# Kernel optimization log

Hardware: AMD Instinct MI355X
Metric: run time of the kernel (lower is better)

The kernel has to match this reference:

```python
import jax, jax.numpy as jnp
import numpy as np

B, S = 4, 16384
D_IN, D_HID, D_KEY, D_VAL, N_HEADS = 512, 2048, 64, 64, 8
SEG_FULL, SAMP = 2048, 4
SEG = SEG_FULL // SAMP  # 512: MoD capacity per segment, also attn segment_len


def setup_inputs() -> dict:
    key = jax.random.key(0)
    ks = jax.random.split(key, 10)
    sc = lambda i, shape: (jax.random.normal(ks[i], shape, jnp.float32) * 0.02)
    return {
        "x": jax.random.normal(ks[0], (B, S, D_IN), jnp.float32),
        "w_samp": sc(1, (D_IN, 1)), "b_samp": jnp.zeros((1,), jnp.float32),
        "w_q": sc(2, (D_IN, N_HEADS * D_KEY)),
        "w_k": sc(3, (D_IN, N_HEADS * D_KEY)),
        "w_v": sc(4, (D_IN, N_HEADS * D_VAL)),
        "w_o": sc(5, (N_HEADS * D_VAL, D_IN)),
        "betas": jax.random.normal(ks[6], (1, N_HEADS, 1, D_VAL), jnp.float32),
        "w1": sc(7, (D_IN, D_HID)), "b1": jnp.zeros((D_HID,), jnp.float32),
        "w2": sc(8, (D_HID, D_IN)), "b2": jnp.zeros((D_IN,), jnp.float32),
    }


def _cm_attention(x, w_q, w_k, w_v, w_o, betas):
    """CompressiveMemory: segment-recurrent linear-attn memory + local softmax attn."""
    b, n, _ = x.shape
    nseg = n // SEG

    def split(w, dh):
        y = (x @ w).reshape(b, n, N_HEADS, dh).transpose(0, 2, 1, 3)          # [b,H,n,dh]
        return y.reshape(b, N_HEADS, nseg, SEG, dh).transpose(2, 0, 1, 3, 4)  # [nseg,b,H,SEG,dh]

    qs, ks_, vs = split(w_q, D_KEY), split(w_k, D_KEY), split(w_v, D_VAL)
    gate = jax.nn.sigmoid(betas)                                              # [1,H,1,dv]
    mem0 = jnp.zeros((b, N_HEADS, D_KEY, D_VAL), x.dtype)
    z0 = jnp.ones((b, N_HEADS, D_KEY, 1), x.dtype) / D_KEY
    scale = D_KEY ** -0.5

    def step(carry, seg):
        mem, z = carry
        q, k, v = seg
        sq = jax.nn.elu(q) + 1.0
        sk = jax.nn.elu(k) + 1.0
        scores = jnp.einsum('bhqk,bhsk->bhqs', q, k) * scale
        att_dot = jax.nn.softmax(scores, axis=-1) @ v                         # [b,H,SEG,dv]
        att_mem = (sq @ mem) / (sq @ z)                                       # uses pre-update mem,z
        mem = mem + jnp.einsum('bhsk,bhsv->bhkv', sk, v)                      # linear update
        z = z + sk.sum(axis=-2)[..., None]
        att = gate * att_mem + (1.0 - gate) * att_dot
        return (mem, z), att

    _, outs = jax.lax.scan(step, (mem0, z0), (qs, ks_, vs))                   # [nseg,b,H,SEG,dv]
    out = outs.transpose(1, 0, 3, 2, 4).reshape(b, n, N_HEADS * D_VAL)
    return out @ w_o


def reference(x, w_samp, b_samp, w_q, w_k, w_v, w_o, betas, w1, b1, w2, b2):
    b, s, d = x.shape
    nseg = s // SEG_FULL
    scores = (x @ w_samp + b_samp)[..., 0]                                    # [B,S]
    # top-SEG tokens per full segment (training-mode routing), kept in sequence order
    seg_scores = scores.reshape(b, nseg, SEG_FULL)
    top = jnp.argsort(-seg_scores, axis=-1)[:, :, :SEG]                       # [B,nseg,SEG]
    sel = jnp.sort(top, axis=-1) + (jnp.arange(nseg) * SEG_FULL)[None, :, None]
    flat = sel.reshape(b, nseg * SEG)                                         # global indices, [B,Ssel]
    x_sel = jnp.take_along_axis(x, flat[..., None], axis=1)                   # gather [B,Ssel,D]
    h = _cm_attention(x_sel, w_q, w_k, w_v, w_o, betas)
    h = jax.nn.gelu(h @ w1 + b1, approximate=False) @ w2 + b2                 # MLP (dropout=0)
    bi = jnp.arange(b)[:, None]
    x_out = x.at[bi, flat].add(h)                                             # scatter-add back
    mask = jnp.zeros((b, s), x.dtype).at[bi, flat].set(1.0)
    # faithful to source: zero positions >= number of selected tokens
    pad = (jnp.arange(s)[None, :] < mask.sum(axis=1)[:, None]).astype(x.dtype)
    x_out = x_out * pad[..., None]
    return x_out, mask.reshape(-1, 1), scores.reshape(-1, 1)
```

## Files before the change

### kernel.cpp

```cpp
#include <hip/hip_runtime.h>
#include <math.h>

#define S_TOT 16384
#define BATCH 4
#define DIN 512
#define NH 8
#define DK 64
#define SEGF 2048
#define SEGS 512
#define NSEG 8
#define NUSE 2
#define MROWS (BATCH*NUSE*SEGS)

typedef unsigned int u32;
typedef __attribute__((ext_vector_type(8))) short short8;
typedef __attribute__((ext_vector_type(4))) float f32x4;

__device__ __forceinline__ short f2b(float f) {
  u32 u = __float_as_uint(f);
  u32 r = u + 0x7fffu + ((u >> 16) & 1u);
  return (short)(r >> 16);
}
__device__ __forceinline__ float b2f(short s) {
  return __uint_as_float(((u32)(unsigned short)s) << 16);
}
__device__ __forceinline__ float b2f_lo(u32 u) { return __uint_as_float(u << 16); }
__device__ __forceinline__ float b2f_hi(u32 u) { return __uint_as_float(u & 0xffff0000u); }

__global__ __launch_bounds__(256) void scores_kernel(
    const float* __restrict__ x, const float* __restrict__ w,
    const float* __restrict__ bsamp, float* __restrict__ out)
{
  int tok  = blockIdx.x * 4 + (threadIdx.x >> 6);
  int lane = threadIdx.x & 63;
  const float4* xr = (const float4*)(x + (size_t)tok * DIN);
  const float4* wr = (const float4*)w;
  float4 a0 = xr[lane],      w0 = wr[lane];
  float4 a1 = xr[lane + 64], w1v = wr[lane + 64];
  float p = a0.x*w0.x + a0.y*w0.y + a0.z*w0.z + a0.w*w0.w
          + a1.x*w1v.x + a1.y*w1v.y + a1.z*w1v.z + a1.w*w1v.w;
  #pragma unroll
  for (int off = 32; off > 0; off >>= 1) p += __shfl_down(p, off);
  if (lane == 0) out[tok] = p + bsamp[0];
}

__global__ __launch_bounds__(256) void topk_rank(
    const float* __restrict__ scores, int* __restrict__ flags,
    float* __restrict__ maskOut)
{
  int c = blockIdx.x & 7, g = (blockIdx.x >> 3) & 7, b = blockIdx.x >> 6;
  __shared__ float sc[SEGF];
  int tid = threadIdx.x;
  const float* src = scores + (size_t)b*S_TOT + (size_t)g*SEGF;
  *(float4*)&sc[tid*8]     = *(const float4*)(src + tid*8);
  *(float4*)&sc[tid*8 + 4] = *(const float4*)(src + tid*8 + 4);
  __syncthreads();
  int i0 = c*256 + tid;
  float mine = sc[i0];
  int cnt = 0;
  #pragma unroll 2
  for (int j = 0; j < SEGF; j += 8) {
    float4 a = *(const float4*)&sc[j];
    float4 d = *(const float4*)&sc[j + 4];
    cnt += (a.x > mine || (a.x == mine && (j+0) < i0)) ? 1 : 0;
    cnt += (a.y > mine || (a.y == mine && (j+1) < i0)) ? 1 : 0;
    cnt += (a.z > mine || (a.z == mine && (j+2) < i0)) ? 1 : 0;
    cnt += (a.w > mine || (a.w == mine && (j+3) < i0)) ? 1 : 0;
    cnt += (d.x > mine || (d.x == mine && (j+4) < i0)) ? 1 : 0;
    cnt += (d.y > mine || (d.y == mine && (j+5) < i0)) ? 1 : 0;
    cnt += (d.z > mine || (d.z == mine && (j+6) < i0)) ? 1 : 0;
    cnt += (d.w > mine || (d.w == mine && (j+7) < i0)) ? 1 : 0;
  }
  int flg = (cnt < SEGS) ? 1 : 0;
  flags[(((b << 3) + g) << 11) + i0] = flg;
  maskOut[(size_t)b*S_TOT + (size_t)g*SEGF + i0] = flg ? 1.0f : 0.0f;
}

__global__ __launch_bounds__(256) void topk_compact(
    const int* __restrict__ flags, int* __restrict__ flat, int* __restrict__ inv)
{
  int g = blockIdx.x & 1, b = blockIdx.x >> 1;
  __shared__ int wsum[4];
  int tid = threadIdx.x;
  int lane = tid & 63, w = tid >> 6;
  const int* f = flags + (((b << 3) + g) << 11);
  int fl[8]; int ls = 0;
  #pragma unroll
  for (int l = 0; l < 8; ++l) { fl[l] = f[tid*8 + l]; ls += fl[l]; }
  int inc = ls;
  #pragma unroll
  for (int off = 1; off < 64; off <<= 1) {
    int t = __shfl_up(inc, off);
    if (lane >= off) inc += t;
  }
  if (lane == 63) wsum[w] = inc;
  __syncthreads();
  int base = 0;
  #pragma unroll
  for (int ww = 0; ww < 4; ++ww) base += (ww < w) ? wsum[ww] : 0;
  int pos = base + inc - ls;
  #pragma unroll
  for (int l = 0; l < 8; ++l) {
    int i = tid*8 + l;
    inv[b*(NUSE*SEGF) + g*SEGF + i] = fl[l] ? (g*SEGS + pos) : -1;
    if (fl[l]) {
      flat[b*(NSEG*SEGS) + g*SEGS + pos] = g*SEGF + i;
      pos++;
    }
  }
}

__global__ __launch_bounds__(256) void transpose_all(
    const float* __restrict__ w_q, const float* __restrict__ w_k,
    const float* __restrict__ w_v, const float* __restrict__ w_o,
    const float* __restrict__ w1,  const float* __restrict__ w2,
    short* __restrict__ Wtqkv, short* __restrict__ Wto,
    short* __restrict__ Wt1,   short* __restrict__ Wt2)
{
  __shared__ float t[32][33];
  int bid = blockIdx.x;
  const float* src; short* dst; int K, N, rowoff, tIdx;
  if (bid < 1024) {
    K = 512; N = 512; tIdx = bid & 255;
    int which = bid >> 8;
    src = which == 0 ? w_q : which == 1 ? w_k : which == 2 ? w_v : w_o;
    dst = which == 3 ? Wto : Wtqkv;
    rowoff = which == 3 ? 0 : which * 512;
  } else if (bid < 2048) {
    K = 512; N = 2048; tIdx = bid - 1024; src = w1; dst = Wt1; rowoff = 0;
  } else {
    K = 2048; N = 512; tIdx = bid - 2048; src = w2; dst = Wt2; rowoff = 0;
  }
  int ntN = N >> 5;
  int n0 = (tIdx % ntN) * 32, k0 = (tIdx / ntN) * 32;
  int tid = threadIdx.x;
  int txx = tid & 31, ty = tid >> 5;
  #pragma unroll
  for (int r = 0; r < 4; ++r)
    t[ty + 8*r][txx] = src[(size_t)(k0 + ty + 8*r) * N + n0 + txx];
  __syncthreads();
  #pragma unroll
  for (int r = 0; r < 4; ++r)
    dst[(size_t)(rowoff + n0 + ty + 8*r) * K + k0 + txx] = f2b(t[txx][ty + 8*r]);
}

__global__ __launch_bounds__(256) void gather_cast(
    const float* __restrict__ x, const int* __restrict__ flat,
    short* __restrict__ xsel)
{
  int tok  = blockIdx.x * 4 + (threadIdx.x >> 6);
  int lane = threadIdx.x & 63;
  int b = tok >> 10, i = tok & 1023;
  int gidx = flat[b * (NSEG*SEGS) + i];
  const float* srcp = x + ((size_t)(b * S_TOT + gidx)) * DIN + lane*8;
  float4 a0 = *(const float4*)srcp;
  float4 a1 = *(const float4*)(srcp + 4);
  uint4 o;
  o.x = (u32)(unsigned short)f2b(a0.x) | ((u32)(unsigned short)f2b(a0.y) << 16);
  o.y = (u32)(unsigned short)f2b(a0.z) | ((u32)(unsigned short)f2b(a0.w) << 16);
  o.z = (u32)(unsigned short)f2b(a1.x) | ((u32)(unsigned short)f2b(a1.y) << 16);
  o.w = (u32)(unsigned short)f2b(a1.z) | ((u32)(unsigned short)f2b(a1.w) << 16);
  *(uint4*)(xsel + (size_t)tok * DIN + lane*8) = o;
}

template<int BM, int BN, int WM, int WN>
__global__ __launch_bounds__(256) void gemm_bf16(
    const short* __restrict__ A, const short* __restrict__ Bt,
    const float* __restrict__ bias, float* __restrict__ Cf,
    short* __restrict__ Cb, short* __restrict__ VtOut, short* __restrict__ KtOut,
    int M, int N, int K, int act)
{
  constexpr int BK = 32;
  constexpr int WAVES_N = BN / WN;
  constexpr int FM = WM / 16, FN = WN / 16;
  __shared__ short Al[2][BM * BK];
  __shared__ short Bl[2][BN * BK];
  const int tid = threadIdx.x;
  const int lane = tid & 63, wid = tid >> 6;
  const int wr = wid / WAVES_N, wc = wid % WAVES_N;
  const int bm = blockIdx.y * BM, bn = blockIdx.x * BN;
  const int srow = tid >> 2;
  const int scol = (tid & 3) * 8;

  f32x4 acc[FM][FN];
  #pragma unroll
  for (int i = 0; i < FM; ++i)
    #pragma unroll
    for (int j = 0; j < FN; ++j)
      #pragma unroll
      for (int e = 0; e < 4; ++e) acc[i][j][e] = 0.f;

  const int NT = K / BK;

  auto stage = [&](int t, int buf) {
    const int k0 = t * BK;
    #pragma unroll
    for (int i = 0; i < BM/64; ++i) {
      const short* gp = A + (size_t)(bm + i*64 + srow) * K + k0 + scol;
      __builtin_amdgcn_global_load_lds(
          (const __attribute__((address_space(1))) void*)gp,
          (__attribute__((address_space(3))) void*)&Al[buf][(i*64 + srow)*BK + scol],
          16, 0, 0);
    }
    #pragma unroll
    for (int i = 0; i < BN/64; ++i) {
      const short* gp = Bt + (size_t)(bn + i*64 + srow) * K + k0 + scol;
      __builtin_amdgcn_global_load_lds(
          (const __attribute__((address_space(1))) void*)gp,
          (__attribute__((address_space(3))) void*)&Bl[buf][(i*64 + srow)*BK + scol],
          16, 0, 0);
    }
  };

  stage(0, 0);
  __syncthreads();
  int cur = 0;
  for (int t = 0; t < NT; ++t) {
    if (t + 1 < NT) stage(t + 1, cur ^ 1);
    short8 af[FM], bf_[FN];
    #pragma unroll
    for (int fm = 0; fm < FM; ++fm)
      af[fm] = *(const short8*)&Al[cur][(wr*WM + fm*16 + (lane & 15))*BK + (lane >> 4)*8];
    #pragma unroll
    for (int fn = 0; fn < FN; ++fn)
      bf_[fn] = *(const short8*)&Bl[cur][(wc*WN + fn*16 + (lane & 15))*BK + (lane >> 4)*8];
    #pragma unroll
    for (int fm = 0; fm < FM; ++fm)
      #pragma unroll
      for (int fn = 0; fn < FN; ++fn)
        acc[fm][fn] = __builtin_amdgcn_mfma_f32_16x16x32_bf16(af[fm], bf_[fn], acc[fm][fn], 0, 0, 0);
    __syncthreads();
    cur ^= 1;
  }

  const int crow0 = (lane >> 4) * 4, ccol = lane & 15;
  #pragma unroll
  for (int fm = 0; fm < FM; ++fm) {
    #pragma unroll
    for (int fn = 0; fn < FN; ++fn) {
      int c = bn + wc*WN + fn*16 + ccol;
      int r0 = bm + wr*WM + fm*16 + crow0;
      float vv[4];
      #pragma unroll
      for (int j = 0; j < 4; ++j) {
        float v = acc[fm][fn][j];
        if (bias) v += bias[c];
        if (act == 1) v = 0.5f * v * (1.0f + erff(v * 0.70710678118f));
        vv[j] = v;
        if (Cf) Cf[(size_t)(r0 + j) * N + c] = v;
        if (Cb) Cb[(size_t)(r0 + j) * N + c] = f2b(v);
      }
      if (VtOut && c >= 1024) {
        int hh = (c - 1024) >> 6, dv = c & 63;
        int bb = r0 >> 10, key = r0 & 1023;
        u32 lo = (u32)(unsigned short)f2b(vv[0]) | ((u32)(unsigned short)f2b(vv[1]) << 16);
        u32 hi = (u32)(unsigned short)f2b(vv[2]) | ((u32)(unsigned short)f2b(vv[3]) << 16);
        *(uint2*)&VtOut[((size_t)((bb*8 + hh)*64 + dv) << 10) + key] = make_uint2(lo, hi);
      }
      if (KtOut && c >= 512 && c < 1024) {
        int hh = (c - 512) >> 6, dk = c & 63;
        int bb = r0 >> 10, key = r0 & 1023;
        float e0 = vv[0] > 0.f ? vv[0] + 1.f : __expf(vv[0]);
        float e1 = vv[1] > 0.f ? vv[1] + 1.f : __expf(vv[1]);
        float e2 = vv[2] > 0.f ? vv[2] + 1.f : __expf(vv[2]);
        float e3 = vv[3] > 0.f ? vv[3] + 1.f : __expf(vv[3]);
        u32 lo = (u32)(unsigned short)f2b(e0) | ((u32)(unsigned short)f2b(e1) << 16);
        u32 hi = (u32)(unsigned short)f2b(e2) | ((u32)(unsigned short)f2b(e3) << 16);
        *(uint2*)&KtOut[((size_t)((bb*8 + hh)*64 + dk) << 10) + key] = make_uint2(lo, hi);
      }
    }
  }
}

__global__ __launch_bounds__(256) void memsum_mfma(
    const short* __restrict__ Kt, const short* __restrict__ Vt,
    short* __restrict__ m0t, float* __restrict__ zf)
{
  int b = blockIdx.x >> 3, h = blockIdx.x & 7;
  const short* ktb = Kt + ((size_t)((b*8+h)*64) << 10);
  const short* vtb = Vt + ((size_t)((b*8+h)*64) << 10);
  int tid = threadIdx.x, lane = tid & 63, w = tid >> 6;
  int ln15 = lane & 15, hi8 = (lane >> 4) * 8;
  f32x4 acc[4];
  #pragma unroll
  for (int nf = 0; nf < 4; ++nf) acc[nf] = (f32x4){0.f,0.f,0.f,0.f};
  #pragma unroll 4
  for (int ks = 0; ks < 16; ++ks) {
    short8 a = *(const short8*)&vtb[(size_t)(w*16 + ln15)*1024 + ks*32 + hi8];
    #pragma unroll
    for (int nf = 0; nf < 4; ++nf) {
      short8 bfr = *(const short8*)&ktb[(size_t)(nf*16 + ln15)*1024 + ks*32 + hi8];
      acc[nf] = __builtin_amdgcn_mfma_f32_16x16x32_bf16(a, bfr, acc[nf], 0, 0, 0);
    }
  }
  size_t mb = (size_t)(b*NH + h) * 4096;
  #pragma unroll
  for (int nf = 0; nf < 4; ++nf)
    #pragma unroll
    for (int j = 0; j < 4; ++j)
      m0t[mb + (size_t)(w*16 + (lane>>4)*4 + j)*64 + nf*16 + ln15] = f2b(acc[nf][j]);
  int row = tid >> 2, q = tid & 3;
  float zs = 0.f;
  #pragma unroll 4
  for (int i = 0; i < 16; ++i) {
    short8 kv = *(const short8*)&ktb[(size_t)row*1024 + q*128 + i*8];
    #pragma unroll
    for (int e = 0; e < 8; ++e) zs += b2f(kv[e]);
  }
  zs += __shfl_xor(zs, 1); zs += __shfl_xor(zs, 2);
  if (q == 0) zf[(b*8+h)*64 + row] = 0.015625f + zs;
}

__global__ __launch_bounds__(256) void attn4(
    const short* __restrict__ qkv, const short* __restrict__ vt,
    const short* __restrict__ m0t, const float* __restrict__ zf,
    const float* __restrict__ betas, short* __restrict__ att)
{
  __shared__ short Qs[64*64];
  __shared__ short Ks[128*64];
  __shared__ short Vts[64*128];
  __shared__ short Ps[4*16*128];
  __shared__ float zl[64];
  __shared__ float relay[64];
  int tid = threadIdx.x, lane = tid & 63, w = tid >> 6;
  int ln15 = lane & 15, hi8 = (lane >> 4) * 8;
  int bx = blockIdx.x;
  int qt = bx & 7, h = (bx >> 3) & 7, g = (bx >> 6) & 1, b = bx >> 7;
  const int seg0 = b*1024 + g*512;
  const int qbase = seg0 + qt*64;

  {
    const short* qg = qkv + (size_t)qbase*1536 + h*64;
    #pragma unroll
    for (int p = 0; p < 2; ++p) {
      int slot = p*256 + tid;
      int row = slot >> 3;
      int off = ((slot & 7)*8) ^ ((row & 7)*8);
      __builtin_amdgcn_global_load_lds(
        (const __attribute__((address_space(1))) void*)(qg + (size_t)row*1536 + off),
        (__attribute__((address_space(3))) void*)&Qs[slot*8], 16, 0, 0);
    }
  }
  if (g && tid < 16) *(float4*)&zl[tid*4] = *(const float4*)(zf + (size_t)(b*8+h)*64 + tid*4);
  __syncthreads();

  short8 qf[2];
  {
    int row = w*16 + ln15;
    #pragma unroll
    for (int ks = 0; ks < 2; ++ks)
      qf[ks] = *(const short8*)&Qs[row*64 + ((ks*32 + hi8) ^ ((row&7)*8))];
  }

  const short* kg = qkv + (size_t)seg0*1536 + 512 + h*64;
  const short* vg = vt + ((size_t)((b*8+h)*64) << 10) + g*512;
  short* Pw = &Ps[w*2048];

  f32x4 oacc[4];
  #pragma unroll
  for (int nf = 0; nf < 4; ++nf) oacc[nf] = (f32x4){0.f,0.f,0.f,0.f};
  float lsum[4] = {0.f,0.f,0.f,0.f};

  for (int c = 0; c < 4; ++c) {
    __syncthreads();
    #pragma unroll
    for (int p = 0; p < 4; ++p) {
      int slot = p*256 + tid;
      int row = slot >> 3;
      int off = ((slot & 7)*8) ^ ((row & 7)*8);
      __builtin_amdgcn_global_load_lds(
        (const __attribute__((address_space(1))) void*)(kg + (size_t)(c*128 + row)*1536 + off),
        (__attribute__((address_space(3))) void*)&Ks[slot*8], 16, 0, 0);
    }
    #pragma unroll
    for (int p = 0; p < 4; ++p) {
      int slot = p*256 + tid;
      int row = slot >> 4;
      int off = ((slot & 15)*8) ^ ((row & 7)*8);
      __builtin_amdgcn_global_load_lds(
        (const __attribute__((address_space(1))) void*)(vg + ((size_t)row << 10) + c*128 + off),
        (__attribute__((address_space(3))) void*)&Vts[slot*8], 16, 0, 0);
    }
    __syncthreads();

    f32x4 sf[8];
    #pragma unroll
    for (int nf = 0; nf < 8; ++nf) sf[nf] = (f32x4){0.f,0.f,0.f,0.f};
    #pragma unroll
    for (int ks = 0; ks < 2; ++ks)
      #pragma unroll
      for (int nf = 0; nf < 8; ++nf) {
        int row = nf*16 + ln15;
        short8 kb = *(const short8*)&Ks[row*64 + ((ks*32 + hi8) ^ ((row&7)*8))];
        sf[nf] = __builtin_amdgcn_mfma_f32_16x16x32_bf16(qf[ks], kb, sf[nf], 0, 0, 0);
      }
    #pragma unroll
    for (int nf = 0; nf < 8; ++nf)
      #pragma unroll
      for (int j = 0; j < 4; ++j) {
        float p = __expf(sf[nf][j] * 0.125f);
        lsum[j] += p;
        int q = (lane >> 4)*4 + j;
        int key = nf*16 + ln15;
        Pw[q*128 + (key ^ ((q&7)*8))] = f2b(p);
      }
    #pragma unroll
    for (int ks = 0; ks < 4; ++ks) {
      short8 pa = *(const short8*)&Pw[ln15*128 + ((ks*32 + hi8) ^ ((ln15&7)*8))];
      #pragma unroll
      for (int nf = 0; nf < 4; ++nf) {
        int row = nf*16 + ln15;
        short8 vb = *(const short8*)&Vts[row*128 + ((ks*32 + hi8) ^ ((row&7)*8))];
        oacc[nf] = __builtin_amdgcn_mfma_f32_16x16x32_bf16(pa, vb, oacc[nf], 0, 0, 0);
      }
    }
  }

  float linv[4];
  #pragma unroll
  for (int j = 0; j < 4; ++j) {
    float s = lsum[j];
    s += __shfl_xor(s, 1); s += __shfl_xor(s, 2);
    s += __shfl_xor(s, 4); s += __shfl_xor(s, 8);
    linv[j] = 1.f / s;
  }

  f32x4 mfr[4];
  #pragma unroll
  for (int nf = 0; nf < 4; ++nf) mfr[nf] = (f32x4){0.f,0.f,0.f,0.f};
  float dinv[4] = {0.f,0.f,0.f,0.f};
  if (g) {
    __syncthreads();
    const short* mg = m0t + (size_t)(b*8+h)*4096;
    #pragma unroll
    for (int p = 0; p < 2; ++p) {
      int slot = p*256 + tid;
      int row = slot >> 3;
      int off = ((slot & 7)*8) ^ ((row & 7)*8);
      __builtin_amdgcn_global_load_lds(
        (const __attribute__((address_space(1))) void*)(mg + (size_t)row*64 + off),
        (__attribute__((address_space(3))) void*)&Ks[slot*8], 16, 0, 0);
    }
    __syncthreads();
    float sqv[2][8]; short8 sqf[2];
    #pragma unroll
    for (int ks = 0; ks < 2; ++ks)
      #pragma unroll
      for (int e = 0; e < 8; ++e) {
        float f = b2f(qf[ks][e]);
        f = f > 0.f ? f + 1.f : __expf(f);
        sqv[ks][e] = f; sqf[ks][e] = f2b(f);
      }
    float denp = 0.f;
    #pragma unroll
    for (int ks = 0; ks < 2; ++ks)
      #pragma unroll
      for (int e = 0; e < 8; ++e) denp += sqv[ks][e] * zl[ks*32 + hi8 + e];
    denp += __shfl_xor(denp, 16); denp += __shfl_xor(denp, 32);
    if (lane < 16) relay[w*16 + lane] = denp;
    #pragma unroll
    for (int ks = 0; ks < 2; ++ks)
      #pragma unroll
      for (int nf = 0; nf < 4; ++nf) {
        int row = nf*16 + ln15;
        short8 mb_ = *(const short8*)&Ks[row*64 + ((ks*32 + hi8) ^ ((row&7)*8))];
        mfr[nf] = __builtin_amdgcn_mfma_f32_16x16x32_bf16(sqf[ks], mb_, mfr[nf], 0, 0, 0);
      }
    #pragma unroll
    for (int j = 0; j < 4; ++j)
      dinv[j] = 1.f / relay[w*16 + (lane>>4)*4 + j];
  }

  #pragma unroll
  for (int nf = 0; nf < 4; ++nf) {
    float bt = betas[h*64 + nf*16 + ln15];
    float gt = 1.f / (1.f + __expf(-bt));
    #pragma unroll
    for (int j = 0; j < 4; ++j) {
      float ad = oacc[nf][j] * linv[j];
      float v = g ? (gt * mfr[nf][j] * dinv[j] + (1.f - gt) * ad) : (1.f - gt) * ad;
      int qrow = qbase + w*16 + (lane>>4)*4 + j;
      att[(size_t)qrow*512 + h*64 + nf*16 + ln15] = f2b(v);
    }
  }
}

__global__ __launch_bounds__(256) void final_kernel(
    const float* __restrict__ x, const int* __restrict__ inv,
    const float* __restrict__ hm, float* __restrict__ outX)
{
  int row  = blockIdx.x * 4 + (threadIdx.x >> 6);
  int lane = threadIdx.x & 63;
  int b = row >> 14;
  int s = row & (S_TOT - 1);
  size_t base = (size_t)row * DIN + lane * 8;
  if (s >= NUSE * SEGF) {
    float4 z = make_float4(0.f,0.f,0.f,0.f);
    *(float4*)(outX + base)     = z;
    *(float4*)(outX + base + 4) = z;
    return;
  }
  float4 a0 = *(const float4*)(x + base);
  float4 a1 = *(const float4*)(x + base + 4);
  int i = inv[b * (NUSE*SEGF) + s];
  if (i >= 0) {
    size_t hb = (size_t)(b * (NUSE*SEGS) + i) * DIN + lane * 8;
    float4 h0 = *(const float4*)(hm + hb);
    float4 h1 = *(const float4*)(hm + hb + 4);
    a0.x += h0.x; a0.y += h0.y; a0.z += h0.z; a0.w += h0.w;
    a1.x += h1.x; a1.y += h1.y; a1.z += h1.z; a1.w += h1.w;
  }
  *(float4*)(outX + base)     = a0;
  *(float4*)(outX + base + 4) = a1;
}

extern "C" void kernel_launch(void* const* d_in, const int* in_sizes, int n_in,
                              void* d_out, int out_size, void* d_ws, size_t ws_size,
                              hipStream_t stream) {
  (void)in_sizes; (void)n_in; (void)out_size; (void)ws_size;
  const float* x      = (const float*)d_in[0];
  const float* w_samp = (const float*)d_in[1];
  const float* b_samp = (const float*)d_in[2];
  const float* w_q    = (const float*)d_in[3];
  const float* w_k    = (const float*)d_in[4];
  const float* w_v    = (const float*)d_in[5];
  const float* w_o    = (const float*)d_in[6];
  const float* betas  = (const float*)d_in[7];
  const float* w1     = (const float*)d_in[8];
  const float* b1     = (const float*)d_in[9];
  const float* w2     = (const float*)d_in[10];
  const float* b2     = (const float*)d_in[11];

  float* outX      = (float*)d_out;
  float* outMask   = outX + (size_t)BATCH * S_TOT * DIN;
  float* outScores = outMask + (size_t)BATCH * S_TOT;

  char* ws = (char*)d_ws;
  int*   flat  = (int*)(ws);
  int*   inv   = (int*)(ws + 65536);
  int*   flags = (int*)(ws + 131072);
  short* M0t   = (short*)(ws + 393216);
  float* Zf    = (float*)(ws + 655360);
  short* Wtqkv = (short*)(ws + 1048576);
  short* Wto   = (short*)(ws + 2621440);
  short* Wt1   = (short*)(ws + 3145728);
  short* Wt2   = (short*)(ws + 5242880);
  short* xsel  = (short*)(ws + 7340032);
  short* qkv   = (short*)(ws + 11534336);
  short* Vt    = (short*)(ws + 24117248);
  short* attb  = (short*)(ws + 28311552);
  short* R0b   = (short*)(ws + 32505856);
  short* Kt    = (short*)(ws + 36700160);
  short* hidB  = (short*)(ws + 7340032);
  float* Hf    = (float*)(ws + 24117248);

  scores_kernel<<<(BATCH*S_TOT)/4, 256, 0, stream>>>(x, w_samp, b_samp, outScores);
  topk_rank<<<BATCH*NSEG*8, 256, 0, stream>>>(outScores, flags, outMask);
  topk_compact<<<BATCH*NUSE, 256, 0, stream>>>(flags, flat, inv);

  transpose_all<<<3072, 256, 0, stream>>>(w_q, w_k, w_v, w_o, w1, w2,
                                          Wtqkv, Wto, Wt1, Wt2);

  gather_cast<<<MROWS/4, 256, 0, stream>>>(x, flat, xsel);

  gemm_bf16<128,128,64,64><<<dim3(12,32), 256, 0, stream>>>(
      xsel, Wtqkv, nullptr, nullptr, qkv, Vt, Kt, MROWS, 1536, 512, 0);

  memsum_mfma<<<BATCH*NH, 256, 0, stream>>>(Kt, Vt, M0t, Zf);
  attn4<<<512, 256, 0, stream>>>(qkv, Vt, M0t, Zf, betas, attb);

  gemm_bf16<64,64,32,32><<<dim3(8,64), 256, 0, stream>>>(
      attb, Wto, nullptr, nullptr, R0b, nullptr, nullptr, MROWS, 512, 512, 0);
  gemm_bf16<128,128,64,64><<<dim3(16,32), 256, 0, stream>>>(
      R0b, Wt1, b1, nullptr, hidB, nullptr, nullptr, MROWS, 2048, 512, 1);
  gemm_bf16<64,64,32,32><<<dim3(8,64), 256, 0, stream>>>(
      hidB, Wt2, b2, Hf, nullptr, nullptr, nullptr, MROWS, 512, 2048, 0);

  final_kernel<<<(BATCH*S_TOT)/4, 256, 0, stream>>>(x, inv, Hf, outX);
}
```

Before: 247.2 us.

## Merge score and weight-transpose kernels, widen GEMM K-tile, simplify attn Q load

Combines the routing-score kernel and the weight transpose/cast kernel into a single launch that branches on block index, removing one launch and letting both run together. The bf16 GEMM K-tile grows from 32 to 64 with two MFMA sub-steps per tile, so there are fewer barriers and the staging loop changes. The attention kernel now loads Q fragments straight from global memory into registers instead of staging them in LDS, dropping a barrier and some LDS use, and it raises wave priority around the MFMA sections. The larger K-tile doubles GEMM LDS use, which may lower occupancy, and the unswizzled 64-wide LDS rows may cause bank conflicts.

Result: no change. 248.7 us (+0.6%).

```diff
diff --git a/kernel.cpp b/kernel.cpp
--- a/kernel.cpp
+++ b/kernel.cpp
@@ -24,24 +24,55 @@
 __device__ __forceinline__ float b2f(short s) {
   return __uint_as_float(((u32)(unsigned short)s) << 16);
 }
-__device__ __forceinline__ float b2f_lo(u32 u) { return __uint_as_float(u << 16); }
-__device__ __forceinline__ float b2f_hi(u32 u) { return __uint_as_float(u & 0xffff0000u); }
-
-__global__ __launch_bounds__(256) void scores_kernel(
+
+__global__ __launch_bounds__(256) void scores_transpose(
     const float* __restrict__ x, const float* __restrict__ w,
-    const float* __restrict__ bsamp, float* __restrict__ out)
-{
-  int tok  = blockIdx.x * 4 + (threadIdx.x >> 6);
-  int lane = threadIdx.x & 63;
-  const float4* xr = (const float4*)(x + (size_t)tok * DIN);
-  const float4* wr = (const float4*)w;
-  float4 a0 = xr[lane],      w0 = wr[lane];
-  float4 a1 = xr[lane + 64], w1v = wr[lane + 64];
-  float p = a0.x*w0.x + a0.y*w0.y + a0.z*w0.z + a0.w*w0.w
-          + a1.x*w1v.x + a1.y*w1v.y + a1.z*w1v.z + a1.w*w1v.w;
-  #pragma unroll
-  for (int off = 32; off > 0; off >>= 1) p += __shfl_down(p, off);
-  if (lane == 0) out[tok] = p + bsamp[0];
+    const float* __restrict__ bsamp, float* __restrict__ out,
+    const float* __restrict__ w_q, const float* __restrict__ w_k,
+    const float* __restrict__ w_v, const float* __restrict__ w_o,
+    const float* __restrict__ w1,  const float* __restrict__ w2,
+    short* __restrict__ Wtqkv, short* __restrict__ Wto,
+    short* __restrict__ Wt1,   short* __restrict__ Wt2)
+{
+  __shared__ float t[32][33];
+  int tid = threadIdx.x;
+  if (blockIdx.x < 16384) {
+    int tok  = blockIdx.x * 4 + (tid >> 6);
+    int lane = tid & 63;
+    const float4* xr = (const float4*)(x + (size_t)tok * DIN);
+    const float4* wr = (const float4*)w;
+    float4 a0 = xr[lane],      w0 = wr[lane];
+    float4 a1 = xr[lane + 64], w1v = wr[lane + 64];
+    float p = a0.x*w0.x + a0.y*w0.y + a0.z*w0.z + a0.w*w0.w
+            + a1.x*w1v.x + a1.y*w1v.y + a1.z*w1v.z + a1.w*w1v.w;
+    #pragma unroll
+    for (int off = 32; off > 0; off >>= 1) p += __shfl_down(p, off);
+    if (lane == 0) out[tok] = p + bsamp[0];
+    return;
+  }
+  int bid = blockIdx.x - 16384;
+  const float* src; short* dst; int K, N, rowoff, tIdx;
+  if (bid < 1024) {
+    K = 512; N = 512; tIdx = bid & 255;
+    int which = bid >> 8;
+    src = which == 0 ? w_q : which == 1 ? w_k : which == 2 ? w_v : w_o;
+    dst = which == 3 ? Wto : Wtqkv;
+    rowoff = which == 3 ? 0 : which * 512;
+  } else if (bid < 2048) {
+    K = 512; N = 2048; tIdx = bid - 1024; src = w1; dst = Wt1; rowoff = 0;
+  } else {
+    K = 2048; N = 512; tIdx = bid - 2048; src = w2; dst = Wt2; rowoff = 0;
+  }
+  int ntN = N >> 5;
+  int n0 = (tIdx % ntN) * 32, k0 = (tIdx / ntN) * 32;
+  int txx = tid & 31, ty = tid >> 5;
+  #pragma unroll
+  for (int r = 0; r < 4; ++r)
+    t[ty + 8*r][txx] = src[(size_t)(k0 + ty + 8*r) * N + n0 + txx];
+  __syncthreads();
+  #pragma unroll
+  for (int r = 0; r < 4; ++r)
+    dst[(size_t)(rowoff + n0 + ty + 8*r) * K + k0 + txx] = f2b(t[txx][ty + 8*r]);
 }
 
 __global__ __launch_bounds__(256) void topk_rank(
@@ -110,40 +141,6 @@
   }
 }
 
-__global__ __launch_bounds__(256) void transpose_all(
-    const float* __restrict__ w_q, const float* __restrict__ w_k,
-    const float* __restrict__ w_v, const float* __restrict__ w_o,
-    const float* __restrict__ w1,  const float* __restrict__ w2,
-    short* __restrict__ Wtqkv, short* __restrict__ Wto,
-    short* __restrict__ Wt1,   short* __restrict__ Wt2)
-{
-  __shared__ float t[32][33];
-  int bid = blockIdx.x;
-  const float* src; short* dst; int K, N, rowoff, tIdx;
-  if (bid < 1024) {
-    K = 512; N = 512; tIdx = bid & 255;
-    int which = bid >> 8;
-    src = which == 0 ? w_q : which == 1 ? w_k : which == 2 ? w_v : w_o;
-    dst = which == 3 ? Wto : Wtqkv;
-    rowoff = which == 3 ? 0 : which * 512;
-  } else if (bid < 2048) {
-    K = 512; N = 2048; tIdx = bid - 1024; src = w1; dst = Wt1; rowoff = 0;
-  } else {
-    K = 2048; N = 512; tIdx = bid - 2048; src = w2; dst = Wt2; rowoff = 0;
-  }
-  int ntN = N >> 5;
-  int n0 = (tIdx % ntN) * 32, k0 = (tIdx / ntN) * 32;
-  int tid = threadIdx.x;
-  int txx = tid & 31, ty = tid >> 5;
-  #pragma unroll
-  for (int r = 0; r < 4; ++r)
-    t[ty + 8*r][txx] = src[(size_t)(k0 + ty + 8*r) * N + n0 + txx];
-  __syncthreads();
-  #pragma unroll
-  for (int r = 0; r < 4; ++r)
-    dst[(size_t)(rowoff + n0 + ty + 8*r) * K + k0 + txx] = f2b(t[txx][ty + 8*r]);
-}
-
 __global__ __launch_bounds__(256) void gather_cast(
     const float* __restrict__ x, const int* __restrict__ flat,
     short* __restrict__ xsel)
@@ -170,7 +167,7 @@
     short* __restrict__ Cb, short* __restrict__ VtOut, short* __restrict__ KtOut,
     int M, int N, int K, int act)
 {
-  constexpr int BK = 32;
+  constexpr int BK = 64;
   constexpr int WAVES_N = BN / WN;
   constexpr int FM = WM / 16, FN = WN / 16;
   __shared__ short Al[2][BM * BK];
@@ -179,8 +176,7 @@
   const int lane = tid & 63, wid = tid >> 6;
   const int wr = wid / WAVES_N, wc = wid % WAVES_N;
   const int bm = blockIdx.y * BM, bn = blockIdx.x * BN;
-  const int srow = tid >> 2;
-  const int scol = (tid & 3) * 8;
+  const int ln15 = lane & 15, hi8 = (lane >> 4) * 8;
 
   f32x4 acc[FM][FN];
   #pragma unroll
@@ -195,19 +191,23 @@
   auto stage = [&](int t, int buf) {
     const int k0 = t * BK;
     #pragma unroll
-    for (int i = 0; i < BM/64; ++i) {
-      const short* gp = A + (size_t)(bm + i*64 + srow) * K + k0 + scol;
+    for (int i = 0; i < BM/32; ++i) {
+      int slot = i*256 + tid;
+      int row = slot >> 3, col = (slot & 7) * 8;
+      const short* gp = A + (size_t)(bm + row) * K + k0 + col;
       __builtin_amdgcn_global_load_lds(
           (const __attribute__((address_space(1))) void*)gp,
-          (__attribute__((address_space(3))) void*)&Al[buf][(i*64 + srow)*BK + scol],
+          (__attribute__((address_space(3))) void*)&Al[buf][row*BK + col],
           16, 0, 0);
     }
     #pragma unroll
-    for (int i = 0; i < BN/64; ++i) {
-      const short* gp = Bt + (size_t)(bn + i*64 + srow) * K + k0 + scol;
+    for (int i = 0; i < BN/32; ++i) {
+      int slot = i*256 + tid;
+      int row = slot >> 3, col = (slot & 7) * 8;
+      const short* gp = Bt + (size_t)(bn + row) * K + k0 + col;
       __builtin_amdgcn_global_load_lds(
           (const __attribute__((address_space(1))) void*)gp,
-          (__attribute__((address_space(3))) void*)&Bl[buf][(i*64 + srow)*BK + scol],
+          (__attribute__((address_space(3))) void*)&Bl[buf][row*BK + col],
           16, 0, 0);
     }
   };
@@ -217,18 +217,21 @@
   int cur = 0;
   for (int t = 0; t < NT; ++t) {
     if (t + 1 < NT) stage(t + 1, cur ^ 1);
-    short8 af[FM], bf_[FN];
-    #pragma unroll
-    for (int fm = 0; fm < FM; ++fm)
-      af[fm] = *(const short8*)&Al[cur][(wr*WM + fm*16 + (lane & 15))*BK + (lane >> 4)*8];
-    #pragma unroll
-    for (int fn = 0; fn < FN; ++fn)
-      bf_[fn] = *(const short8*)&Bl[cur][(wc*WN + fn*16 + (lane & 15))*BK + (lane >> 4)*8];
-    #pragma unroll
-    for (int fm = 0; fm < FM; ++fm)
+    #pragma unroll
+    for (int ks = 0; ks < 2; ++ks) {
+      short8 af[FM], bf_[FN];
+      #pragma unroll
+      for (int fm = 0; fm < FM; ++fm)
+        af[fm] = *(const short8*)&Al[cur][(wr*WM + fm*16 + ln15)*BK + ks*32 + hi8];
       #pragma unroll
       for (int fn = 0; fn < FN; ++fn)
-        acc[fm][fn] = __builtin_amdgcn_mfma_f32_16x16x32_bf16(af[fm], bf_[fn], acc[fm][fn], 0, 0, 0);
+        bf_[fn] = *(const short8*)&Bl[cur][(wc*WN + fn*16 + ln15)*BK + ks*32 + hi8];
+      #pragma unroll
+      for (int fm = 0; fm < FM; ++fm)
+        #pragma unroll
+        for (int fn = 0; fn < FN; ++fn)
+          acc[fm][fn] = __builtin_amdgcn_mfma_f32_16x16x32_bf16(af[fm], bf_[fn], acc[fm][fn], 0, 0, 0);
+    }
     __syncthreads();
     cur ^= 1;
   }
@@ -316,7 +319,6 @@
     const short* __restrict__ m0t, const float* __restrict__ zf,
     const float* __restrict__ betas, short* __restrict__ att)
 {
-  __shared__ short Qs[64*64];
   __shared__ short Ks[128*64];
   __shared__ short Vts[64*128];
   __shared__ short Ps[4*16*128];
@@ -329,28 +331,13 @@
   const int seg0 = b*1024 + g*512;
   const int qbase = seg0 + qt*64;
 
-  {
-    const short* qg = qkv + (size_t)qbase*1536 + h*64;
-    #pragma unroll
-    for (int p = 0; p < 2; ++p) {
-      int slot = p*256 + tid;
-      int row = slot >> 3;
-      int off = ((slot & 7)*8) ^ ((row & 7)*8);
-      __builtin_amdgcn_global_load_lds(
-        (const __attribute__((address_space(1))) void*)(qg + (size_t)row*1536 + off),
-        (__attribute__((address_space(3))) void*)&Qs[slot*8], 16, 0, 0);
-    }
-  }
-  if (g && tid < 16) *(float4*)&zl[tid*4] = *(const float4*)(zf + (size_t)(b*8+h)*64 + tid*4);
-  __syncthreads();
-
   short8 qf[2];
   {
-    int row = w*16 + ln15;
-    #pragma unroll
-    for (int ks = 0; ks < 2; ++ks)
-      qf[ks] = *(const short8*)&Qs[row*64 + ((ks*32 + hi8) ^ ((row&7)*8))];
-  }
+    const short* qg = qkv + (size_t)(qbase + w*16 + ln15)*1536 + h*64;
+    qf[0] = *(const short8*)(qg + hi8);
+    qf[1] = *(const short8*)(qg + 32 + hi8);
+  }
+  if (g && tid < 16) *(float4*)&zl[tid*4] = *(const float4*)(zf + (size_t)(b*8+h)*64 + tid*4);
 
   const short* kg = qkv + (size_t)seg0*1536 + 512 + h*64;
   const short* vg = vt + ((size_t)((b*8+h)*64) << 10) + g*512;
@@ -386,6 +373,7 @@
     f32x4 sf[8];
     #pragma unroll
     for (int nf = 0; nf < 8; ++nf) sf[nf] = (f32x4){0.f,0.f,0.f,0.f};
+    __builtin_amdgcn_s_setprio(1);
     #pragma unroll
     for (int ks = 0; ks < 2; ++ks)
       #pragma unroll
@@ -394,6 +382,7 @@
         short8 kb = *(const short8*)&Ks[row*64 + ((ks*32 + hi8) ^ ((row&7)*8))];
         sf[nf] = __builtin_amdgcn_mfma_f32_16x16x32_bf16(qf[ks], kb, sf[nf], 0, 0, 0);
       }
+    __builtin_amdgcn_s_setprio(0);
     #pragma unroll
     for (int nf = 0; nf < 8; ++nf)
       #pragma unroll
@@ -404,6 +393,7 @@
         int key = nf*16 + ln15;
         Pw[q*128 + (key ^ ((q&7)*8))] = f2b(p);
       }
+    __builtin_amdgcn_s_setprio(1);
     #pragma unroll
     for (int ks = 0; ks < 4; ++ks) {
       short8 pa = *(const short8*)&Pw[ln15*128 + ((ks*32 + hi8) ^ ((ln15&7)*8))];
@@ -414,6 +404,7 @@
         oacc[nf] = __builtin_amdgcn_mfma_f32_16x16x32_bf16(pa, vb, oacc[nf], 0, 0, 0);
       }
     }
+    __builtin_amdgcn_s_setprio(0);
   }
 
   float linv[4];
@@ -554,12 +545,11 @@
   short* hidB  = (short*)(ws + 7340032);
   float* Hf    = (float*)(ws + 24117248);
 
-  scores_kernel<<<(BATCH*S_TOT)/4, 256, 0, stream>>>(x, w_samp, b_samp, outScores);
+  scores_transpose<<<16384 + 3072, 256, 0, stream>>>(
+      x, w_samp, b_samp, outScores,
+      w_q, w_k, w_v, w_o, w1, w2, Wtqkv, Wto, Wt1, Wt2);
   topk_rank<<<BATCH*NSEG*8, 256, 0, stream>>>(outScores, flags, outMask);
   topk_compact<<<BATCH*NUSE, 256, 0, stream>>>(flags, flat, inv);
-
-  transpose_all<<<3072, 256, 0, stream>>>(w_q, w_k, w_v, w_o, w1, w2,
-                                          Wtqkv, Wto, Wt1, Wt2);
 
   gather_cast<<<MROWS/4, 256, 0, stream>>>(x, flat, xsel);
 
```
